# Kernel optimization log

Measured on AMD Instinct MI355X. Metric: run time of the kernel, lower is better.

Reference implementation:

```python
import jax, jax.numpy as jnp
import numpy as np

HIDDEN = 512
EMBED = 512
VOCAB = 32000
BRANCH = 4
LEVELS = 9  # level 0 = root, level LEVELS-1 = leaves (complete 4-ary tree)
N_NODES = sum(BRANCH ** l for l in range(LEVELS))  # 87381


def setup_inputs() -> dict:
    key = jax.random.key(0)
    ks = jax.random.split(key, 16)
    s = 1.0 / np.sqrt(HIDDEN)
    inp = {
        "token_ids": jax.random.randint(ks[0], (N_NODES,), 0, VOCAB, dtype=jnp.int32),
        "emb": jax.random.normal(ks[1], (VOCAB, EMBED), jnp.float32) * 0.02,
        "Wi": jax.random.normal(ks[2], (EMBED, HIDDEN), jnp.float32) * s,
        "Ui": jax.random.normal(ks[3], (HIDDEN, HIDDEN), jnp.float32) * s,
        "bi": jnp.zeros((HIDDEN,), jnp.float32),
        "Wf": jax.random.normal(ks[4], (EMBED, HIDDEN), jnp.float32) * s,
        "Uf": jax.random.normal(ks[5], (HIDDEN, HIDDEN), jnp.float32) * s,
        "bf": jnp.zeros((HIDDEN,), jnp.float32),
        "Wo": jax.random.normal(ks[6], (EMBED, HIDDEN), jnp.float32) * s,
        "Uo": jax.random.normal(ks[7], (HIDDEN, HIDDEN), jnp.float32) * s,
        "bo": jnp.zeros((HIDDEN,), jnp.float32),
        "Wu": jax.random.normal(ks[8], (EMBED, HIDDEN), jnp.float32) * s,
        "Uu": jax.random.normal(ks[9], (HIDDEN, HIDDEN), jnp.float32) * s,
        "bu": jnp.zeros((HIDDEN,), jnp.float32),
        "branching": BRANCH,
        "n_levels": LEVELS,
    }
    return inp


def reference(token_ids, emb, Wi, Ui, bi, Wf, Uf, bf, Wo, Uo, bo, Wu, Uu, bu,
              branching, n_levels):
    # Level-synchronous Child-Sum Tree-LSTM over a complete `branching`-ary tree.
    # token_ids is laid out level by level, root first.
    B = int(branching)
    L = int(n_levels)
    H = Wi.shape[1]
    level_sizes = [B ** l for l in range(L)]
    offsets = np.concatenate([[0], np.cumsum(level_sizes)])  # static Python ints

    # Leaves: original code sets h = c = 0 (leaf embedding is computed but unused).
    h = jnp.zeros((level_sizes[-1], H), dtype=emb.dtype)
    c = jnp.zeros((level_sizes[-1], H), dtype=emb.dtype)
    hs_levels = [h]  # hidden states collected leaves -> root (level order)

    for l in range(L - 2, -1, -1):
        n = level_sizes[l]
        x = jnp.take(emb, token_ids[offsets[l]:offsets[l + 1]], axis=0)  # [n, E]
        ch_h = h.reshape(n, B, H)  # children of node k are contiguous
        ch_c = c.reshape(n, B, H)
        h_tilde = ch_h.sum(axis=1)  # [n, H] child-sum
        i = jax.nn.sigmoid(x @ Wi + h_tilde @ Ui + bi)
        # per-child forget gates: [n, B, H]
        f = jax.nn.sigmoid((x @ Wf + bf)[:, None, :] + ch_h @ Uf)
        o = jax.nn.sigmoid(x @ Wo + h_tilde @ Uo + bo)
        u = jnp.tanh(x @ Wu + h_tilde @ Uu + bu)
        c = i * u + (f * ch_c).sum(axis=1)
        h = o * jnp.tanh(c)
        hs_levels.append(h)

    hidden_states = jnp.concatenate(hs_levels, axis=0)  # [N_NODES, H]
    return hidden_states, h, c  # h, c are the root states, shape [1, H]
```

## Files before the change

kernel.cpp:

```cpp
#include <hip/hip_runtime.h>

#define DI __device__ __forceinline__

typedef __attribute__((ext_vector_type(8))) __bf16 bf16x8;
typedef __attribute__((ext_vector_type(4))) float f32x4;
typedef __attribute__((ext_vector_type(8))) unsigned short ushort8;
typedef unsigned long long ull;

static DI unsigned short f2b(float f) {
  unsigned int x = __builtin_bit_cast(unsigned int, f);
  unsigned int r = (x + 0x7FFFu + ((x >> 16) & 1u)) >> 16;
  return (unsigned short)r;
}
static DI float b2f(unsigned short u) {
  return __builtin_bit_cast(float, (unsigned int)u << 16);
}
static DI float sigmf(float x) { return 1.0f / (1.0f + __expf(-x)); }

typedef const __attribute__((address_space(1))) void* gcptr;
typedef __attribute__((address_space(3))) void* lptr;
static DI void gl_lds16(const void* g, void* l) {
  __builtin_amdgcn_global_load_lds((gcptr)g, (lptr)l, 16, 0, 0);
}

#define GCOL(g, d) ((((d) >> 4) << 6) + ((g) << 4) + ((d) & 15))

static DI size_t qaddr(int NT, int row4, int c) {
  int tm = row4 >> 5, tn = c >> 7;
  int rq = row4 & 31, c7 = c & 127;
  int wv = ((rq >> 4) << 1) | (c7 >> 6);
  int mf = (rq >> 2) & 3, nf = (c7 >> 4) & 3;
  int lane = ((rq & 3) << 4) | (c7 & 15);
  return ((size_t)(tm * NT + tn) << 12) + (size_t)((((wv << 4) + (mf << 2) + nf) << 6) + lane);
}

__global__ void prep_pack(const float* __restrict__ Wi, const float* __restrict__ Ui,
                          const float* __restrict__ bi, const float* __restrict__ Wf,
                          const float* __restrict__ Uf, const float* __restrict__ bfv,
                          const float* __restrict__ Wo, const float* __restrict__ Uo,
                          const float* __restrict__ bo, const float* __restrict__ Wu,
                          const float* __restrict__ Uu, const float* __restrict__ bu,
                          unsigned short* __restrict__ Wp, unsigned short* __restrict__ Upiou,
                          unsigned short* __restrict__ Upf, float* __restrict__ bias)
{
  int u = blockIdx.x * blockDim.x + threadIdx.x;
  if (u < 131072) {
    int k8 = u >> 11, n = u & 2047;
    int gate = (n >> 4) & 3;
    int d = ((n >> 6) << 4) | (n & 15);
    const float* W = (gate == 0) ? Wi : (gate == 1) ? Wf : (gate == 2) ? Wo : Wu;
    ushort8 pk;
    #pragma unroll
    for (int t = 0; t < 8; ++t) pk[t] = f2b(W[(size_t)(k8*8+t)*512 + d]);
    *(ushort8*)&Wp[(size_t)u*8] = pk;
  } else if (u < 131072 + 98304) {
    int v = u - 131072;
    int k8 = v / 1536, n = v - k8*1536;
    const float* U = (n < 512) ? Ui : (n < 1024) ? Uo : Uu;
    int c = n & 511;
    ushort8 pk;
    #pragma unroll
    for (int t = 0; t < 8; ++t) pk[t] = f2b(U[(size_t)(k8*8+t)*512 + c]);
    *(ushort8*)&Upiou[(size_t)v*8] = pk;
  } else {
    int v = u - 229376;
    int k8 = v >> 9, c = v & 511;
    ushort8 pk;
    #pragma unroll
    for (int t = 0; t < 8; ++t) pk[t] = f2b(Uf[(size_t)(k8*8+t)*512 + c]);
    *(ushort8*)&Upf[(size_t)v*8] = pk;
  }
  if (u < 2048) {
    int gate = (u >> 4) & 3;
    int d = ((u >> 6) << 4) | (u & 15);
    bias[u] = (gate == 0) ? bi[d] : (gate == 1) ? bfv[d] : (gate == 2) ? bo[d] : bu[d];
  }
}

__global__ void gather_x(const int* __restrict__ tok, const float* __restrict__ emb,
                         unsigned short* __restrict__ X)
{
  int u = blockIdx.x * blockDim.x + threadIdx.x;
  if (u >= 22272*64) return;
  int R = u >> 6, ch = u & 63;
  int l, node;
  if (R < 512)       { l = R >> 7; node = R & 127; int sz = 1 << (2*l); if (node >= sz) node = sz - 1; }
  else if (R < 768)  { l = 4; node = R - 512; }
  else if (R < 1792) { l = 5; node = R - 768; }
  else if (R < 5888) { l = 6; node = R - 1792; }
  else               { l = 7; node = R - 5888; }
  static const int offs_c[8] = {0,1,5,21,85,341,1365,5461};
  int tk = tok[offs_c[l] + node];
  const float* src = emb + (size_t)tk*512 + ch*8;
  ushort8 pk;
  #pragma unroll
  for (int t = 0; t < 8; ++t) pk[t] = f2b(src[t]);
  *(ushort8*)&X[(size_t)u*8] = pk;
}

struct GDesc {
  const unsigned short* A;
  const unsigned short* Bp;
  ull* C;
  int M, N, NT;
};
struct L7P {
  float* hout; unsigned short* hb; float* cb; unsigned short* ht;
  float* zbase; size_t z4;
};

template<bool FUSED>
__global__ __launch_bounds__(256)
void gemm512(GDesc g1, GDesc g2, int split, const float* __restrict__ bias, L7P l7)
{
  __shared__ unsigned short As[2*128*32];
  __shared__ unsigned short Bs[2*4*128*8];

  const int nwg = gridDim.x, orig = blockIdx.x;
  const int q = nwg >> 3, r = nwg & 7;
  const int xcd = orig & 7, idx = orig >> 3;
  const int wg = (xcd < r ? xcd*(q+1) : r*(q+1) + (xcd-r)*q) + idx;

  const bool role1 = (wg < split);
  GDesc g = role1 ? g1 : g2;
  const int lwg = role1 ? wg : wg - split;
  const int tm = lwg / g.NT, tn = lwg - tm * g.NT;

  const int tid = threadIdx.x;
  const int wave = tid >> 6, lane = tid & 63;
  const int Mbase = tm * 128, Nbase = tn * 128;
  const int wr = wave >> 1, wc = wave & 1;

  f32x4 acc[4][4] = {};

  auto STAGE = [&](int p, int k0) {
    #pragma unroll
    for (int c = 0; c < 2; ++c) {
      int lrow = c*64 + wave*16 + (lane >> 2);
      int grow = Mbase + lrow; if (grow >= g.M) grow = g.M - 1;
      gl_lds16(g.A + (size_t)grow*512 + k0 + (((lane & 3) ^ (lrow & 3)) * 8),
               As + p*(128*32) + (c*64 + wave*16)*32);
    }
    #pragma unroll
    for (int c = 0; c < 2; ++c) {
      gl_lds16(g.Bp + ((size_t)((k0 >> 3) + wave) * g.N + Nbase + c*64 + lane) * 8,
               Bs + p*(4*128*8) + (wave*128 + c*64)*8);
    }
  };

  auto COMPUTE = [&](int p) {
    bf16x8 af[4], bfr[4];
    #pragma unroll
    for (int mf = 0; mf < 4; ++mf) {
      int row = wr*64 + mf*16 + (lane & 15);
      int kc  = lane >> 4;
      af[mf] = *(const bf16x8*)&As[p*(128*32) + row*32 + ((kc ^ (row & 3)) * 8)];
    }
    #pragma unroll
    for (int nf = 0; nf < 4; ++nf) {
      int col = wc*64 + nf*16 + (lane & 15);
      int k8  = lane >> 4;
      bfr[nf] = *(const bf16x8*)&Bs[p*(4*128*8) + (k8*128 + col) * 8];
    }
    #pragma unroll
    for (int mf = 0; mf < 4; ++mf)
      #pragma unroll
      for (int nf = 0; nf < 4; ++nf)
        acc[mf][nf] = __builtin_amdgcn_mfma_f32_16x16x32_bf16(af[mf], bfr[nf], acc[mf][nf], 0, 0, 0);
  };

  STAGE(0, 0);
  __syncthreads();
  #pragma unroll
  for (int it = 0; it < 15; ++it) {
    STAGE((it + 1) & 1, (it + 1) * 32);
    COMPUTE(it & 1);
    __syncthreads();
  }
  COMPUTE(1);

  auto ZERO_DUTY = [&]() {
    if constexpr (FUSED) {
      size_t b4 = (size_t)orig * 3072;
      f32x4 z = {0.f, 0.f, 0.f, 0.f};
      f32x4* zp = (f32x4*)l7.zbase;
      #pragma unroll
      for (int i = 0; i < 12; ++i) {
        size_t off = b4 + (size_t)i*256 + tid;
        if (off < l7.z4) zp[off] = z;
      }
    }
  };

  if (FUSED && tm >= 46) {
    const int dlow = lane & 15;
    const float bi_ = bias[Nbase + wc*64      + dlow];
    const float bo_ = bias[Nbase + wc*64 + 32 + dlow];
    const float bu_ = bias[Nbase + wc*64 + 48 + dlow];
    const int d = tn*32 + wc*16 + dlow;
    #pragma unroll
    for (int mf = 0; mf < 4; ++mf) {
      int node0 = Mbase - 5888 + wr*64 + mf*16 + (lane >> 4)*4;
      float hts = 0.f;
      #pragma unroll
      for (int rr = 0; rr < 4; ++rr) {
        float iv = sigmf(acc[mf][0][rr] + bi_);
        float ov = sigmf(acc[mf][2][rr] + bo_);
        float uv = tanhf(acc[mf][3][rr] + bu_);
        float cv = iv * uv;
        float hv = ov * tanhf(cv);
        size_t node = node0 + rr;
        l7.hout[node*512 + d] = hv;
        l7.hb[node*512 + d]   = f2b(hv);
        l7.cb[node*512 + d]   = cv;
        hts += hv;
      }
      l7.ht[(size_t)(node0 >> 2)*512 + d] = f2b(hts);
    }
    ZERO_DUTY();
  } else {
    ZERO_DUTY();
    float bv[4];
    #pragma unroll
    for (int nf = 0; nf < 4; ++nf)
      bv[nf] = (bias != nullptr && role1) ? bias[Nbase + wc*64 + nf*16 + (lane & 15)] : 0.f;
    ull* Cb = g.C + ((size_t)(tm * g.NT + tn) << 12) + ((size_t)wave << 10);
    #pragma unroll
    for (int mf = 0; mf < 4; ++mf)
      #pragma unroll
      for (int nf = 0; nf < 4; ++nf) {
        f32x4 a = acc[mf][nf];
        ull pk = (ull)f2b(a[0] + bv[nf]) | ((ull)f2b(a[1] + bv[nf]) << 16)
               | ((ull)f2b(a[2] + bv[nf]) << 32) | ((ull)f2b(a[3] + bv[nf]) << 48);
        Cb[(mf*4 + nf)*64 + lane] = pk;
      }
  }
}

__global__ __launch_bounds__(256)
void combine2(const ull* __restrict__ Gq,
              const ull* __restrict__ Rq,
              const ull* __restrict__ Fq,
              const float* __restrict__ cch,
              float* __restrict__ hout,
              unsigned short* __restrict__ hbf,
              float* __restrict__ cout,
              unsigned short* __restrict__ htout,
              float* __restrict__ rootx,
              int n)
{
  const int b = blockIdx.x, t = threadIdx.x;
  #pragma unroll
  for (int half = 0; half < 2; ++half) {
    const int c = t + half * 256;
    ull gi4 = Gq[qaddr(16, b, GCOL(0, c))];
    ull gf4 = Gq[qaddr(16, b, GCOL(1, c))];
    ull go4 = Gq[qaddr(16, b, GCOL(2, c))];
    ull gu4 = Gq[qaddr(16, b, GCOL(3, c))];
    ull ri4 = Rq[qaddr(12, b, c)];
    ull ro4 = Rq[qaddr(12, b, c + 512)];
    ull ru4 = Rq[qaddr(12, b, c + 1024)];
    float hts = 0.f;
    #pragma unroll
    for (int rI = 0; rI < 4; ++rI) {
      int j = b*4 + rI;
      float gi = b2f((unsigned short)(gi4 >> (16*rI)));
      float gf = b2f((unsigned short)(gf4 >> (16*rI)));
      float go = b2f((unsigned short)(go4 >> (16*rI)));
      float gu = b2f((unsigned short)(gu4 >> (16*rI)));
      float iv = sigmf(gi + b2f((unsigned short)(ri4 >> (16*rI))));
      float ov = sigmf(go + b2f((unsigned short)(ro4 >> (16*rI))));
      float uv = tanhf(gu + b2f((unsigned short)(ru4 >> (16*rI))));
      ull f4 = Fq[qaddr(4, j, c)];
      const float* cc = cch + (size_t)(j*4)*512 + c;
      float fs = 0.f;
      #pragma unroll
      for (int k = 0; k < 4; ++k)
        fs += sigmf(gf + b2f((unsigned short)(f4 >> (16*k)))) * cc[(size_t)k*512];
      float cv = iv*uv + fs;
      float hv = ov * tanhf(cv);
      if (j < n) {
        hout[(size_t)j*512 + c] = hv;
        hbf[(size_t)j*512 + c]  = f2b(hv);
        cout[(size_t)j*512 + c] = cv;
        if (rootx && j == 0) { rootx[c] = hv; rootx[512 + c] = cv; }
        hts += hv;
      }
    }
    if (htout) htout[(size_t)b*512 + c] = f2b(hts);
  }
}

extern "C" void kernel_launch(void* const* d_in, const int* in_sizes, int n_in,
                              void* d_out, int out_size, void* d_ws, size_t ws_size,
                              hipStream_t stream)
{
  const int*   tok = (const int*)d_in[0];
  const float* emb = (const float*)d_in[1];
  const float* Wi  = (const float*)d_in[2];
  const float* Ui  = (const float*)d_in[3];
  const float* bi  = (const float*)d_in[4];
  const float* Wf  = (const float*)d_in[5];
  const float* Uf  = (const float*)d_in[6];
  const float* bfv = (const float*)d_in[7];
  const float* Wo  = (const float*)d_in[8];
  const float* Uo  = (const float*)d_in[9];
  const float* bo  = (const float*)d_in[10];
  const float* Wu  = (const float*)d_in[11];
  const float* Uu  = (const float*)d_in[12];
  const float* bu  = (const float*)d_in[13];

  char* ws = (char*)d_ws;
  unsigned short* Wp    = (unsigned short*)(ws + 0);
  unsigned short* Upiou = (unsigned short*)(ws + 2097152);
  unsigned short* Upf   = (unsigned short*)(ws + 3670016);
  float*          bias  = (float*)        (ws + 4194304);
  unsigned short* hbf   = (unsigned short*)(ws + 4202496);
  unsigned short* htbf  = (unsigned short*)(ws + 26571776);
  float*          cbuf  = (float*)        (ws + 32163840);
  ull*            RiouQ = (ull*)          (ws + 76902400);
  ull*            RfQ   = (ull*)          (ws + 89485312);
  ull*            Gq    = (ull*)          (ws + 106262528);
  unsigned short* X     = (unsigned short*)(ws + 130379776);

  float* fout = (float*)d_out;

  static const int  offs[9]    = {0,1,5,21,85,341,1365,5461,21845};
  static const int  padbase[8] = {0,128,256,384,512,768,1792,5888};
  static const long outoff[8]  = {87380,87376,87360,87296,87040,86016,81920,65536};

  prep_pack<<<1024, 256, 0, stream>>>(Wi,Ui,bi,Wf,Uf,bfv,Wo,Uo,bo,Wu,Uu,bu,
                                      Wp,Upiou,Upf,bias);
  gather_x<<<(22272*64)/256, 256, 0, stream>>>(tok, emb, X);

  GDesc gA { X, Wp, Gq, 22272, 2048, 16 };
  L7P l7 { fout + (size_t)outoff[7]*512, hbf + (size_t)offs[7]*512,
           cbuf + (size_t)offs[7]*512, htbf + (size_t)offs[6]*512,
           fout, (size_t)65536*512/4 };
  gemm512<true><<<174*16, 256, 0, stream>>>(gA, gA, 174*16, bias, l7);

  L7P l7n {};
  for (int l = 6; l >= 0; --l) {
    int n = 1 << (2*l);
    int tm1 = (n + 127) / 128, tm2 = (4*n + 127) / 128;
    int split = tm1 * 12;
    GDesc g1 { htbf + (size_t)offs[l]*512,   Upiou, RiouQ, n,   1536, 12 };
    GDesc g2 { hbf  + (size_t)offs[l+1]*512, Upf,   RfQ,   4*n, 512,  4  };
    gemm512<false><<<split + tm2*4, 256, 0, stream>>>(g1, g2, split, nullptr, l7n);
    combine2<<<(n + 3) / 4, 256, 0, stream>>>(
        Gq + (size_t)padbase[l]*512, RiouQ, RfQ, cbuf + (size_t)offs[l+1]*512,
        fout + (size_t)outoff[l]*512, hbf + (size_t)offs[l]*512, cbuf + (size_t)offs[l]*512,
        (l > 0) ? htbf + (size_t)offs[l-1]*512 : nullptr,
        (l == 0) ? fout + (size_t)87381*512 : nullptr,
        n);
  }
}
```

Baseline: 307.1 us.

## Make GEMM persistent with cross-tile prefetch and new LDS swizzle

```diff
diff --git a/kernel.cpp b/kernel.cpp
--- a/kernel.cpp
+++ b/kernel.cpp
@@ -108,53 +108,65 @@
   float* hout; unsigned short* hb; float* cb; unsigned short* ht;
   float* zbase; size_t z4;
 };
+struct TD {
+  const unsigned short* A; const unsigned short* Bp; ull* C;
+  int M, N, NT, tm, tn; bool role1;
+};
+
+static DI void decode(const GDesc& g1, const GDesc& g2, int split, int idx, TD& t) {
+  bool r1 = idx < split;
+  const GDesc& g = r1 ? g1 : g2;
+  int l = r1 ? idx : idx - split;
+  t.tm = l / g.NT; t.tn = l - t.tm * g.NT;
+  t.A = g.A; t.Bp = g.Bp; t.C = g.C; t.M = g.M; t.N = g.N; t.NT = g.NT; t.role1 = r1;
+}
 
 template<bool FUSED>
-__global__ __launch_bounds__(256)
-void gemm512(GDesc g1, GDesc g2, int split, const float* __restrict__ bias, L7P l7)
+__global__ __launch_bounds__(256, 4)
+void gemm512(GDesc g1, GDesc g2, int split, int total, const float* __restrict__ bias, L7P l7)
 {
   __shared__ unsigned short As[2*128*32];
   __shared__ unsigned short Bs[2*4*128*8];
 
-  const int nwg = gridDim.x, orig = blockIdx.x;
-  const int q = nwg >> 3, r = nwg & 7;
+  const int grid = gridDim.x, orig = blockIdx.x;
+  const int q = grid >> 3, r = grid & 7;
   const int xcd = orig & 7, idx = orig >> 3;
   const int wg = (xcd < r ? xcd*(q+1) : r*(q+1) + (xcd-r)*q) + idx;
 
-  const bool role1 = (wg < split);
-  GDesc g = role1 ? g1 : g2;
-  const int lwg = role1 ? wg : wg - split;
-  const int tm = lwg / g.NT, tn = lwg - tm * g.NT;
+  const int q2 = total / grid, r2 = total - q2*grid;
+  const int lo = wg*q2 + (wg < r2 ? wg : r2);
+  const int hi = lo + q2 + (wg < r2 ? 1 : 0);
+  if (lo >= hi) return;
 
   const int tid = threadIdx.x;
   const int wave = tid >> 6, lane = tid & 63;
-  const int Mbase = tm * 128, Nbase = tn * 128;
   const int wr = wave >> 1, wc = wave & 1;
 
-  f32x4 acc[4][4] = {};
-
-  auto STAGE = [&](int p, int k0) {
+  auto STAGE = [&](int p, const TD& t, int k0) {
     #pragma unroll
     for (int c = 0; c < 2; ++c) {
       int lrow = c*64 + wave*16 + (lane >> 2);
-      int grow = Mbase + lrow; if (grow >= g.M) grow = g.M - 1;
-      gl_lds16(g.A + (size_t)grow*512 + k0 + (((lane & 3) ^ (lrow & 3)) * 8),
+      int grow = t.tm*128 + lrow; if (grow >= t.M) grow = t.M - 1;
+      int srcch = (lane & 3) ^ ((lrow >> 1) & 3);
+      gl_lds16(t.A + (size_t)grow*512 + k0 + srcch*8,
                As + p*(128*32) + (c*64 + wave*16)*32);
     }
     #pragma unroll
     for (int c = 0; c < 2; ++c) {
-      gl_lds16(g.Bp + ((size_t)((k0 >> 3) + wave) * g.N + Nbase + c*64 + lane) * 8,
+      gl_lds16(t.Bp + ((size_t)((k0 >> 3) + wave) * t.N + t.tn*128 + c*64 + lane) * 8,
                Bs + p*(4*128*8) + (wave*128 + c*64)*8);
     }
   };
 
+  f32x4 acc[4][4];
+  bf16x8 af[4], bfr[4];
+
   auto COMPUTE = [&](int p) {
-    bf16x8 af[4], bfr[4];
     #pragma unroll
     for (int mf = 0; mf < 4; ++mf) {
       int row = wr*64 + mf*16 + (lane & 15);
       int kc  = lane >> 4;
-      af[mf] = *(const bf16x8*)&As[p*(128*32) + row*32 + ((kc ^ (row & 3)) * 8)];
+      af[mf] = *(const bf16x8*)&As[p*(128*32) + row*32 + ((kc ^ ((row >> 1) & 3)) * 8)];
     }
     #pragma unroll
     for (int nf = 0; nf < 4; ++nf) {
@@ -169,71 +181,84 @@
         acc[mf][nf] = __builtin_amdgcn_mfma_f32_16x16x32_bf16(af[mf], bfr[nf], acc[mf][nf], 0, 0, 0);
   };
 
-  STAGE(0, 0);
+  TD cur, nxt;
+  decode(g1, g2, split, lo, cur);
+  STAGE(0, cur, 0);
   __syncthreads();
-  #pragma unroll
-  for (int it = 0; it < 15; ++it) {
-    STAGE((it + 1) & 1, (it + 1) * 32);
-    COMPUTE(it & 1);
-    __syncthreads();
-  }
-  COMPUTE(1);
-
-  auto ZERO_DUTY = [&]() {
-    if constexpr (FUSED) {
-      size_t b4 = (size_t)orig * 3072;
-      f32x4 z = {0.f, 0.f, 0.f, 0.f};
-      f32x4* zp = (f32x4*)l7.zbase;
-      #pragma unroll
-      for (int i = 0; i < 12; ++i) {
-        size_t off = b4 + (size_t)i*256 + tid;
-        if (off < l7.z4) zp[off] = z;
+  int pp = 0;
+
+  for (int ti = lo; ti < hi; ++ti) {
+    const bool have_next = (ti + 1 < hi);
+    if (have_next) decode(g1, g2, split, ti + 1, nxt);
+    #pragma unroll
+    for (int mf = 0; mf < 4; ++mf)
+      #pragma unroll
+      for (int nf = 0; nf < 4; ++nf)
+        acc[mf][nf] = f32x4{0.f, 0.f, 0.f, 0.f};
+
+    #pragma unroll
+    for (int it = 0; it < 16; ++it) {
+      if (it < 15)            STAGE(pp ^ 1, cur, (it + 1) * 32);
+      else if (have_next)     STAGE(pp ^ 1, nxt, 0);
+      COMPUTE(pp);
+      __syncthreads();
+      pp ^= 1;
+    }
+
+    if (FUSED && cur.tm >= 46) {
+      const int dlow = lane & 15;
+      const int Nb = cur.tn * 128;
+      const float bi_ = bias[Nb + wc*64      + dlow];
+      const float bo_ = bias[Nb + wc*64 + 32 + dlow];
+      const float bu_ = bias[Nb + wc*64 + 48 + dlow];
+      const int d = cur.tn*32 + wc*16 + dlow;
+      #pragma unroll
+      for (int mf = 0; mf < 4; ++mf) {
+        int node0 = cur.tm*128 - 5888 + wr*64 + mf*16 + (lane >> 4)*4;
+        float hts = 0.f;
+        #pragma unroll
+        for (int rr = 0; rr < 4; ++rr) {
+          float iv = sigmf(acc[mf][0][rr] + bi_);
+          float ov = sigmf(acc[mf][2][rr] + bo_);
+          float uv = tanhf(acc[mf][3][rr] + bu_);
+          float cv = iv * uv;
+          float hv = ov * tanhf(cv);
+          size_t node = node0 + rr;
+          l7.hout[node*512 + d] = hv;
+          l7.hb[node*512 + d]   = f2b(hv);
+          l7.cb[node*512 + d]   = cv;
+          hts += hv;
+        }
+        l7.ht[(size_t)(node0 >> 2)*512 + d] = f2b(hts);
       }
-    }
-  };
-
-  if (FUSED && tm >= 46) {
-    const int dlow = lane & 15;
-    const float bi_ = bias[Nbase + wc*64      + dlow];
-    const float bo_ = bias[Nbase + wc*64 + 32 + dlow];
-    const float bu_ = bias[Nbase + wc*64 + 48 + dlow];
-    const int d = tn*32 + wc*16 + dlow;
-    #pragma unroll
-    for (int mf = 0; mf < 4; ++mf) {
-      int node0 = Mbase - 5888 + wr*64 + mf*16 + (lane >> 4)*4;
-      float hts = 0.f;
-      #pragma unroll
-      for (int rr = 0; rr < 4; ++rr) {
-        float iv = sigmf(acc[mf][0][rr] + bi_);
-        float ov = sigmf(acc[mf][2][rr] + bo_);
-        float uv = tanhf(acc[mf][3][rr] + bu_);
-        float cv = iv * uv;
-        float hv = ov * tanhf(cv);
-        size_t node = node0 + rr;
-        l7.hout[node*512 + d] = hv;
-        l7.hb[node*512 + d]   = f2b(hv);
-        l7.cb[node*512 + d]   = cv;
-        hts += hv;
-      }
-      l7.ht[(size_t)(node0 >> 2)*512 + d] = f2b(hts);
-    }
-    ZERO_DUTY();
-  } else {
-    ZERO_DUTY();
-    float bv[4];
-    #pragma unroll
-    for (int nf = 0; nf < 4; ++nf)
-      bv[nf] = (bias != nullptr && role1) ? bias[Nbase + wc*64 + nf*16 + (lane & 15)] : 0.f;
-    ull* Cb = g.C + ((size_t)(tm * g.NT + tn) << 12) + ((size_t)wave << 10);
-    #pragma unroll
-    for (int mf = 0; mf < 4; ++mf)
-      #pragma unroll
-      for (int nf = 0; nf < 4; ++nf) {
-        f32x4 a = acc[mf][nf];
-        ull pk = (ull)f2b(a[0] + bv[nf]) | ((ull)f2b(a[1] + bv[nf]) << 16)
-               | ((ull)f2b(a[2] + bv[nf]) << 32) | ((ull)f2b(a[3] + bv[nf]) << 48);
-        Cb[(mf*4 + nf)*64 + lane] = pk;
-      }
+    } else {
+      float bv[4];
+      #pragma unroll
+      for (int nf = 0; nf < 4; ++nf)
+        bv[nf] = (bias != nullptr && cur.role1) ? bias[cur.tn*128 + wc*64 + nf*16 + (lane & 15)] : 0.f;
+      ull* Cb = cur.C + ((size_t)(cur.tm * cur.NT + cur.tn) << 12) + ((size_t)wave << 10);
+      #pragma unroll
+      for (int mf = 0; mf < 4; ++mf)
+        #pragma unroll
+        for (int nf = 0; nf < 4; ++nf) {
+          f32x4 a = acc[mf][nf];
+          ull pk = (ull)f2b(a[0] + bv[nf]) | ((ull)f2b(a[1] + bv[nf]) << 16)
+                 | ((ull)f2b(a[2] + bv[nf]) << 32) | ((ull)f2b(a[3] + bv[nf]) << 48);
+          Cb[(mf*4 + nf)*64 + lane] = pk;
+        }
+    }
+    cur = nxt;
+  }
+
+  if constexpr (FUSED) {
+    size_t b4 = (size_t)orig * 8192;
+    f32x4 z = {0.f, 0.f, 0.f, 0.f};
+    f32x4* zp = (f32x4*)l7.zbase;
+    #pragma unroll 4
+    for (int i = 0; i < 32; ++i) {
+      size_t off = b4 + (size_t)i*256 + tid;
+      if (off < l7.z4) zp[off] = z;
+    }
   }
 }
 
@@ -337,16 +362,18 @@
   L7P l7 { fout + (size_t)outoff[7]*512, hbf + (size_t)offs[7]*512,
            cbuf + (size_t)offs[7]*512, htbf + (size_t)offs[6]*512,
            fout, (size_t)65536*512/4 };
-  gemm512<true><<<174*16, 256, 0, stream>>>(gA, gA, 174*16, bias, l7);
+  gemm512<true><<<1024, 256, 0, stream>>>(gA, gA, 174*16, 174*16, bias, l7);
 
   L7P l7n {};
   for (int l = 6; l >= 0; --l) {
     int n = 1 << (2*l);
     int tm1 = (n + 127) / 128, tm2 = (4*n + 127) / 128;
     int split = tm1 * 12;
+    int total = split + tm2 * 4;
+    int grid  = total < 1024 ? total : 1024;
     GDesc g1 { htbf + (size_t)offs[l]*512,   Upiou, RiouQ, n,   1536, 12 };
     GDesc g2 { hbf  + (size_t)offs[l+1]*512, Upf,   RfQ,   4*n, 512,  4  };
-    gemm512<false><<<split + tm2*4, 256, 0, stream>>>(g1, g2, split, nullptr, l7n);
+    gemm512<false><<<grid, 256, 0, stream>>>(g1, g2, split, total, nullptr, l7n);
     combine2<<<(n + 3) / 4, 256, 0, stream>>>(
         Gq + (size_t)padbase[l]*512, RiouQ, RfQ, cbuf + (size_t)offs[l+1]*512,
         fout + (size_t)outoff[l]*512, hbf + (size_t)offs[l]*512, cbuf + (size_t)offs[l]*512,
```

Result: slower. 369.6 us (+20.4%).

## Pre-swizzle GEMM operands into MFMA panels and load fragments directly without LDS

Applied to the files above, without the earlier changes.

```diff
diff --git a/kernel.cpp b/kernel.cpp
--- a/kernel.cpp
+++ b/kernel.cpp
@@ -17,13 +17,11 @@
 }
 static DI float sigmf(float x) { return 1.0f / (1.0f + __expf(-x)); }
 
-typedef const __attribute__((address_space(1))) void* gcptr;
-typedef __attribute__((address_space(3))) void* lptr;
-static DI void gl_lds16(const void* g, void* l) {
-  __builtin_amdgcn_global_load_lds((gcptr)g, (lptr)l, 16, 0, 0);
-}
-
 #define GCOL(g, d) ((((d) >> 4) << 6) + ((g) << 4) + ((d) & 15))
+
+static DI size_t pidx(int row, int kchunk) {
+  return ((size_t)(row >> 4) * 64 + kchunk) * 128 + (size_t)(row & 15) * 8;
+}
 
 static DI size_t qaddr(int NT, int row4, int c) {
   int tm = row4 >> 5, tn = c >> 7;
@@ -95,7 +93,7 @@
   ushort8 pk;
   #pragma unroll
   for (int t = 0; t < 8; ++t) pk[t] = f2b(src[t]);
-  *(ushort8*)&X[(size_t)u*8] = pk;
+  *(ushort8*)&X[pidx(R, ch)] = pk;
 }
 
 struct GDesc {
@@ -110,12 +108,9 @@
 };
 
 template<bool FUSED>
-__global__ __launch_bounds__(256)
-void gemm512(GDesc g1, GDesc g2, int split, const float* __restrict__ bias, L7P l7)
-{
-  __shared__ unsigned short As[2*128*32];
-  __shared__ unsigned short Bs[2*4*128*8];
-
+__global__ __launch_bounds__(256, 3)
+void gemm_direct(GDesc g1, GDesc g2, int split, const float* __restrict__ bias, L7P l7)
+{
   const int nwg = gridDim.x, orig = blockIdx.x;
   const int q = nwg >> 3, r = nwg & 7;
   const int xcd = orig & 7, idx = orig >> 3;
@@ -128,58 +123,77 @@
 
   const int tid = threadIdx.x;
   const int wave = tid >> 6, lane = tid & 63;
+  const int wr = wave >> 1, wc = wave & 1;
+  const int l15 = lane & 15, l4 = lane >> 4;
   const int Mbase = tm * 128, Nbase = tn * 128;
-  const int wr = wave >> 1, wc = wave & 1;
+
+  unsigned int a0[4], b0[4];
+  #pragma unroll
+  for (int mf = 0; mf < 4; ++mf) {
+    int row = Mbase + wr*64 + mf*16 + l15;
+    if (row >= g.M) row = g.M - 1;
+    a0[mf] = (unsigned int)(((row >> 4) * 64 + l4) * 128 + (row & 15) * 8);
+  }
+  #pragma unroll
+  for (int nf = 0; nf < 4; ++nf)
+    b0[nf] = (unsigned int)(((size_t)l4 * g.N + Nbase + wc*64 + nf*16 + l15) * 8);
+  const unsigned int bstep = (unsigned int)g.N * 32;
 
   f32x4 acc[4][4] = {};
 
-  auto STAGE = [&](int p, int k0) {
-    #pragma unroll
-    for (int c = 0; c < 2; ++c) {
-      int lrow = c*64 + wave*16 + (lane >> 2);
-      int grow = Mbase + lrow; if (grow >= g.M) grow = g.M - 1;
-      gl_lds16(g.A + (size_t)grow*512 + k0 + (((lane & 3) ^ (lrow & 3)) * 8),
-               As + p*(128*32) + (c*64 + wave*16)*32);
+  #define LDA(dst, ks) { _Pragma("unroll") for (int mf = 0; mf < 4; ++mf)      \
+      dst[mf] = *(const bf16x8*)(g.A + a0[mf] + (ks)*512u); }
+  #define LDB(dst, ks) { _Pragma("unroll") for (int nf = 0; nf < 4; ++nf)      \
+      dst[nf] = *(const bf16x8*)(g.Bp + b0[nf] + (ks)*bstep); }
+  #define MM(af_, bf_) { _Pragma("unroll") for (int mf = 0; mf < 4; ++mf)      \
+      _Pragma("unroll") for (int nf = 0; nf < 4; ++nf)                         \
+        acc[mf][nf] = __builtin_amdgcn_mfma_f32_16x16x32_bf16(                 \
+            af_[mf], bf_[nf], acc[mf][nf], 0, 0, 0); }
+
+  bf16x8 aA[4], bA[4], aB[4], bB[4];
+  LDA(aA, 0u); LDB(bA, 0u);
+  #pragma unroll
+  for (int ks = 0; ks < 16; ks += 2) {
+    if (ks + 1 < 16) { LDA(aB, (unsigned)(ks+1)); LDB(bB, (unsigned)(ks+1)); }
+    MM(aA, bA);
+    if (ks + 2 < 16) { LDA(aA, (unsigned)(ks+2)); LDB(bA, (unsigned)(ks+2)); }
+    if (ks + 1 < 16) MM(aB, bB);
+  }
+
+  if (FUSED && tm >= 46) {
+    const float bi_ = bias[Nbase + wc*64      + l15];
+    const float bo_ = bias[Nbase + wc*64 + 32 + l15];
+    const float bu_ = bias[Nbase + wc*64 + 48 + l15];
+    const int d = tn*32 + wc*16 + l15;
+    #pragma unroll
+    for (int mf = 0; mf < 4; ++mf) {
+      int node0 = Mbase - 5888 + wr*64 + mf*16 + l4*4;
+      float hts = 0.f;
+      #pragma unroll
+      for (int rr = 0; rr < 4; ++rr) {
+        float iv = sigmf(acc[mf][0][rr] + bi_);
+        float ov = sigmf(acc[mf][2][rr] + bo_);
+        float uv = tanhf(acc[mf][3][rr] + bu_);
+        float cv = iv * uv;
+        float hv = ov * tanhf(cv);
+        int node = node0 + rr;
+        l7.hout[(size_t)node*512 + d] = hv;
+        l7.hb[pidx(node, d >> 3) + (d & 7)] = f2b(hv);
+        l7.cb[(size_t)node*512 + d] = cv;
+        hts += hv;
+      }
+      int pr = node0 >> 2;
+      l7.ht[pidx(pr, d >> 3) + (d & 7)] = f2b(hts);
     }
-    #pragma unroll
-    for (int c = 0; c < 2; ++c) {
-      gl_lds16(g.Bp + ((size_t)((k0 >> 3) + wave) * g.N + Nbase + c*64 + lane) * 8,
-               Bs + p*(4*128*8) + (wave*128 + c*64)*8);
+    size_t b4 = (size_t)orig * 3072;
+    f32x4 z = {0.f, 0.f, 0.f, 0.f};
+    f32x4* zp = (f32x4*)l7.zbase;
+    #pragma unroll
+    for (int i = 0; i < 12; ++i) {
+      size_t off = b4 + (size_t)i*256 + tid;
+      if (off < l7.z4) zp[off] = z;
     }
-  };
-
-  auto COMPUTE = [&](int p) {
-    bf16x8 af[4], bfr[4];
-    #pragma unroll
-    for (int mf = 0; mf < 4; ++mf) {
-      int row = wr*64 + mf*16 + (lane & 15);
-      int kc  = lane >> 4;
-      af[mf] = *(const bf16x8*)&As[p*(128*32) + row*32 + ((kc ^ (row & 3)) * 8)];
-    }
-    #pragma unroll
-    for (int nf = 0; nf < 4; ++nf) {
-      int col = wc*64 + nf*16 + (lane & 15);
-      int k8  = lane >> 4;
-      bfr[nf] = *(const bf16x8*)&Bs[p*(4*128*8) + (k8*128 + col) * 8];
-    }
-    #pragma unroll
-    for (int mf = 0; mf < 4; ++mf)
-      #pragma unroll
-      for (int nf = 0; nf < 4; ++nf)
-        acc[mf][nf] = __builtin_amdgcn_mfma_f32_16x16x32_bf16(af[mf], bfr[nf], acc[mf][nf], 0, 0, 0);
-  };
-
-  STAGE(0, 0);
-  __syncthreads();
-  #pragma unroll
-  for (int it = 0; it < 15; ++it) {
-    STAGE((it + 1) & 1, (it + 1) * 32);
-    COMPUTE(it & 1);
-    __syncthreads();
-  }
-  COMPUTE(1);
-
-  auto ZERO_DUTY = [&]() {
+  } else {
     if constexpr (FUSED) {
       size_t b4 = (size_t)orig * 3072;
       f32x4 z = {0.f, 0.f, 0.f, 0.f};
@@ -190,40 +204,10 @@
         if (off < l7.z4) zp[off] = z;
       }
     }
-  };
-
-  if (FUSED && tm >= 46) {
-    const int dlow = lane & 15;
-    const float bi_ = bias[Nbase + wc*64      + dlow];
-    const float bo_ = bias[Nbase + wc*64 + 32 + dlow];
-    const float bu_ = bias[Nbase + wc*64 + 48 + dlow];
-    const int d = tn*32 + wc*16 + dlow;
-    #pragma unroll
-    for (int mf = 0; mf < 4; ++mf) {
-      int node0 = Mbase - 5888 + wr*64 + mf*16 + (lane >> 4)*4;
-      float hts = 0.f;
-      #pragma unroll
-      for (int rr = 0; rr < 4; ++rr) {
-        float iv = sigmf(acc[mf][0][rr] + bi_);
-        float ov = sigmf(acc[mf][2][rr] + bo_);
-        float uv = tanhf(acc[mf][3][rr] + bu_);
-        float cv = iv * uv;
-        float hv = ov * tanhf(cv);
-        size_t node = node0 + rr;
-        l7.hout[node*512 + d] = hv;
-        l7.hb[node*512 + d]   = f2b(hv);
-        l7.cb[node*512 + d]   = cv;
-        hts += hv;
-      }
-      l7.ht[(size_t)(node0 >> 2)*512 + d] = f2b(hts);
-    }
-    ZERO_DUTY();
-  } else {
-    ZERO_DUTY();
     float bv[4];
     #pragma unroll
     for (int nf = 0; nf < 4; ++nf)
-      bv[nf] = (bias != nullptr && role1) ? bias[Nbase + wc*64 + nf*16 + (lane & 15)] : 0.f;
+      bv[nf] = (bias != nullptr && role1) ? bias[Nbase + wc*64 + nf*16 + l15] : 0.f;
     ull* Cb = g.C + ((size_t)(tm * g.NT + tn) << 12) + ((size_t)wave << 10);
     #pragma unroll
     for (int mf = 0; mf < 4; ++mf)
@@ -281,13 +265,13 @@
       float hv = ov * tanhf(cv);
       if (j < n) {
         hout[(size_t)j*512 + c] = hv;
-        hbf[(size_t)j*512 + c]  = f2b(hv);
+        hbf[pidx(j, c >> 3) + (c & 7)] = f2b(hv);
         cout[(size_t)j*512 + c] = cv;
         if (rootx && j == 0) { rootx[c] = hv; rootx[512 + c] = cv; }
         hts += hv;
       }
     }
-    if (htout) htout[(size_t)b*512 + c] = f2b(hts);
+    if (htout) htout[pidx(b, c >> 3) + (c & 7)] = f2b(hts);
   }
 }
 
@@ -316,17 +300,19 @@
   unsigned short* Upf   = (unsigned short*)(ws + 3670016);
   float*          bias  = (float*)        (ws + 4194304);
   unsigned short* hbf   = (unsigned short*)(ws + 4202496);
-  unsigned short* htbf  = (unsigned short*)(ws + 26571776);
-  float*          cbuf  = (float*)        (ws + 32163840);
-  ull*            RiouQ = (ull*)          (ws + 76902400);
-  ull*            RfQ   = (ull*)          (ws + 89485312);
-  ull*            Gq    = (ull*)          (ws + 106262528);
-  unsigned short* X     = (unsigned short*)(ws + 130379776);
+  unsigned short* htbf  = (unsigned short*)(ws + 26599424);
+  float*          cbuf  = (float*)        (ws + 32219136);
+  ull*            RiouQ = (ull*)          (ws + 76957696);
+  ull*            RfQ   = (ull*)          (ws + 89540608);
+  ull*            Gq    = (ull*)          (ws + 106317824);
+  unsigned short* X     = (unsigned short*)(ws + 130435072);
 
   float* fout = (float*)d_out;
 
   static const int  offs[9]    = {0,1,5,21,85,341,1365,5461,21845};
   static const int  padbase[8] = {0,128,256,384,512,768,1792,5888};
+  static const int  hpan[8]    = {0,16,32,48,112,368,1392,5488};
+  static const int  tpan[7]    = {0,16,32,48,112,368,1392};
   static const long outoff[8]  = {87380,87376,87360,87296,87040,86016,81920,65536};
 
   prep_pack<<<1024, 256, 0, stream>>>(Wi,Ui,bi,Wf,Uf,bfv,Wo,Uo,bo,Wu,Uu,bu,
@@ -334,23 +320,24 @@
   gather_x<<<(22272*64)/256, 256, 0, stream>>>(tok, emb, X);
 
   GDesc gA { X, Wp, Gq, 22272, 2048, 16 };
-  L7P l7 { fout + (size_t)outoff[7]*512, hbf + (size_t)offs[7]*512,
-           cbuf + (size_t)offs[7]*512, htbf + (size_t)offs[6]*512,
+  L7P l7 { fout + (size_t)outoff[7]*512, hbf + (size_t)hpan[7]*512,
+           cbuf + (size_t)offs[7]*512, htbf + (size_t)tpan[6]*512,
            fout, (size_t)65536*512/4 };
-  gemm512<true><<<174*16, 256, 0, stream>>>(gA, gA, 174*16, bias, l7);
+  gemm_direct<true><<<174*16, 256, 0, stream>>>(gA, gA, 174*16, bias, l7);
 
   L7P l7n {};
   for (int l = 6; l >= 0; --l) {
     int n = 1 << (2*l);
     int tm1 = (n + 127) / 128, tm2 = (4*n + 127) / 128;
     int split = tm1 * 12;
-    GDesc g1 { htbf + (size_t)offs[l]*512,   Upiou, RiouQ, n,   1536, 12 };
-    GDesc g2 { hbf  + (size_t)offs[l+1]*512, Upf,   RfQ,   4*n, 512,  4  };
-    gemm512<false><<<split + tm2*4, 256, 0, stream>>>(g1, g2, split, nullptr, l7n);
+    int total = split + tm2 * 4;
+    GDesc g1 { htbf + (size_t)tpan[l]*512,   Upiou, RiouQ, n,   1536, 12 };
+    GDesc g2 { hbf  + (size_t)hpan[l+1]*512, Upf,   RfQ,   4*n, 512,  4  };
+    gemm_direct<false><<<total, 256, 0, stream>>>(g1, g2, split, nullptr, l7n);
     combine2<<<(n + 3) / 4, 256, 0, stream>>>(
         Gq + (size_t)padbase[l]*512, RiouQ, RfQ, cbuf + (size_t)offs[l+1]*512,
-        fout + (size_t)outoff[l]*512, hbf + (size_t)offs[l]*512, cbuf + (size_t)offs[l]*512,
-        (l > 0) ? htbf + (size_t)offs[l-1]*512 : nullptr,
+        fout + (size_t)outoff[l]*512, hbf + (size_t)hpan[l]*512, cbuf + (size_t)offs[l]*512,
+        (l > 0) ? htbf + (size_t)tpan[l-1]*512 : nullptr,
         (l == 0) ? fout + (size_t)87381*512 : nullptr,
         n);
   }
```

Result: no change. 308.8 us (+0.6%).
